# Performance work log

Measured on AMD Instinct MI355X. Metric: run time of the kernel, lower is better.

## Reference

```python
import jax, jax.numpy as jnp
import numpy as np

B, T, C = 2, 2048, 1024
H = 16
DH = C // H  # 64
EPS = 1e-5


def setup_inputs() -> dict:
    key = jax.random.key(0)
    ks = jax.random.split(key, 12)
    s = lambda k, shape, fan: jax.random.normal(k, shape, jnp.float32) / np.sqrt(fan)
    return {
        'x': jax.random.normal(ks[0], (B, T, C), jnp.float32),
        'wq': s(ks[1], (H, C, DH), C),
        'wk': s(ks[2], (H, C, DH), C),
        'wv': s(ks[3], (H, C, DH), C),
        'w_proj': s(ks[4], (C, C), C),
        'b_proj': jnp.zeros((C,), jnp.float32),
        'g_ln1': jnp.ones((C,), jnp.float32),
        'b_ln1': jnp.zeros((C,), jnp.float32),
        'g_ln2': jnp.ones((C,), jnp.float32),
        'b_ln2': jnp.zeros((C,), jnp.float32),
        'w_ff1': s(ks[5], (C, 4 * C), C),
        'b_ff1': jnp.zeros((4 * C,), jnp.float32),
        'w_ff2': s(ks[6], (4 * C, C), 4 * C),
        'b_ff2': jnp.zeros((C,), jnp.float32),
    }


def _layernorm(x, g, b):
    mu = jnp.mean(x, axis=-1, keepdims=True)
    var = jnp.mean(jnp.square(x - mu), axis=-1, keepdims=True)
    return (x - mu) * jax.lax.rsqrt(var + EPS) * g + b


def _attention(x, wq, wk, wv, w_proj, b_proj):
    # per-head projections, batched over heads: [B,T,C] x [H,C,Dh] -> [B,H,T,Dh]
    q = jnp.einsum('btc,hcd->bhtd', x, wq)
    k = jnp.einsum('btc,hcd->bhtd', x, wk)
    v = jnp.einsum('btc,hcd->bhtd', x, wv)
    scores = jnp.einsum('bhtd,bhsd->bhts', q, k) / np.sqrt(DH).astype(np.float32)
    t = x.shape[1]
    causal = jnp.tril(jnp.ones((t, t), bool))
    scores = jnp.where(causal, scores, -jnp.inf)
    w = jax.nn.softmax(scores, axis=-1)
    out = jnp.einsum('bhts,bhsd->bhtd', w, v)  # [B,H,T,Dh]
    # concat heads (head order matches torch cat over head list)
    out = out.transpose(0, 2, 1, 3).reshape(x.shape[0], t, C)
    return out @ w_proj + b_proj


def reference(x, wq, wk, wv, w_proj, b_proj, g_ln1, b_ln1, g_ln2, b_ln2, w_ff1, b_ff1, w_ff2, b_ff2):
    x = x + _attention(_layernorm(x, g_ln1, b_ln1), wq, wk, wv, w_proj, b_proj)
    h = _layernorm(x, g_ln2, b_ln2)
    ff = jax.nn.relu(h @ w_ff1 + b_ff1) @ w_ff2 + b_ff2
    return x + ff
```

## Files before the change

### kernel.cpp

```cpp
#include <hip/hip_runtime.h>

#define DEV __device__ __forceinline__

typedef __attribute__((ext_vector_type(4))) float f32x4;
typedef __attribute__((ext_vector_type(8))) short short8;
typedef __attribute__((ext_vector_type(8))) __bf16 bf16x8;

DEV unsigned short f2bf(float f) {
  __bf16 h = (__bf16)f;
  return __builtin_bit_cast(unsigned short, h);
}
DEV unsigned pack2(float a, float b) {
  return (unsigned)f2bf(a) | ((unsigned)f2bf(b) << 16);
}
DEV bf16x8 ld_bf8(const unsigned short* p) {
  short8 v = *(const short8*)p;
  return __builtin_bit_cast(bf16x8, v);
}
DEV f32x4 MFMA(bf16x8 a, bf16x8 b, f32x4 c) {
  return __builtin_amdgcn_mfma_f32_16x16x32_bf16(a, b, c, 0, 0, 0);
}

typedef const __attribute__((address_space(1))) void GV;
typedef __attribute__((address_space(3))) void LV;
DEV void gl_lds16(const void* g, void* l) {
  __builtin_amdgcn_global_load_lds((GV*)g, (LV*)l, 16, 0, 0);
}

DEV void xcd_decode(int gx, int& bx, int& by) {
  const int nwg = gridDim.x, bid = blockIdx.x;
  const int cpx = nwg >> 3;
  const int swz = (bid & 7) * cpx + (bid >> 3);
  by = swz / gx;
  bx = swz % gx;
}

template<int RX, int RY, int RCOLS>
DEV void xcd_decode2(int& bx, int& by) {
  const int bid = blockIdx.x;
  const int xcd = bid & 7, local = bid >> 3;
  bx = (xcd % RCOLS) * RX + (local % RX);
  by = (xcd / RCOLS) * RY + (local / RX);
}

__global__ void __launch_bounds__(256) ln_fused(
    const float* __restrict__ x, const float* __restrict__ g,
    const float* __restrict__ b, unsigned short* __restrict__ y)
{
  const int row = blockIdx.x, tid = threadIdx.x;
  const float4 xv = ((const float4*)(x + (size_t)row * 1024))[tid];
  float s  = xv.x + xv.y + xv.z + xv.w;
  float s2 = xv.x * xv.x + xv.y * xv.y + xv.z * xv.z + xv.w * xv.w;
#pragma unroll
  for (int o = 32; o > 0; o >>= 1) { s += __shfl_down(s, o); s2 += __shfl_down(s2, o); }
  __shared__ float ps[4], ps2[4];
  if ((tid & 63) == 0) { ps[tid >> 6] = s; ps2[tid >> 6] = s2; }
  __syncthreads();
  float S  = ps[0] + ps[1] + ps[2] + ps[3];
  float S2 = ps2[0] + ps2[1] + ps2[2] + ps2[3];
  float mu = S * (1.f / 1024.f);
  float rs = rsqrtf(S2 * (1.f / 1024.f) - mu * mu + 1e-5f);
  const float4 gv = ((const float4*)g)[tid];
  const float4 bv = ((const float4*)b)[tid];
  uint2 r;
  r.x = pack2((xv.x - mu) * rs * gv.x + bv.x, (xv.y - mu) * rs * gv.y + bv.y);
  r.y = pack2((xv.z - mu) * rs * gv.z + bv.z, (xv.w - mu) * rs * gv.w + bv.w);
  ((uint2*)(y + (size_t)row * 1024))[tid] = r;
}

__global__ void __launch_bounds__(256) transp_f2b(
    const float* __restrict__ src, unsigned short* __restrict__ dst, int R, int C)
{
  __shared__ float t[64][65];
  const int c0 = blockIdx.x * 64, r0 = blockIdx.y * 64;
  const int tx = threadIdx.x & 63, tq = threadIdx.x >> 6;
#pragma unroll
  for (int i = 0; i < 16; i++) {
    int r = tq * 16 + i;
    t[r][tx] = src[(size_t)(r0 + r) * C + c0 + tx];
  }
  __syncthreads();
#pragma unroll
  for (int i = 0; i < 16; i++) {
    int c = tq * 16 + i;
    dst[(size_t)(c0 + c) * R + r0 + tx] = f2bf(t[tx][c]);
  }
}

__global__ void __launch_bounds__(256) qkv_transp(
    const float* __restrict__ wq, const float* __restrict__ wk,
    const float* __restrict__ wv, unsigned short* __restrict__ dst)
{
  __shared__ float t[64][65];
  const int c0 = blockIdx.x * 64, h = blockIdx.y, z = blockIdx.z;
  const float* w = (z == 0 ? wq : z == 1 ? wk : wv) + (size_t)h * 1024 * 64;
  const int tx = threadIdx.x & 63, tq = threadIdx.x >> 6;
#pragma unroll
  for (int i = 0; i < 16; i++) {
    int c = tq * 16 + i;
    t[c][tx] = w[(size_t)(c0 + c) * 64 + tx];
  }
  __syncthreads();
  unsigned short* drow = dst + (size_t)(z * 1024 + h * 64) * 1024 + c0;
#pragma unroll
  for (int i = 0; i < 16; i++) {
    int d = tq * 16 + i;
    drow[(size_t)d * 1024 + tx] = f2bf(t[tx][d]);
  }
}

__global__ void __launch_bounds__(256) v_transp(
    const unsigned short* __restrict__ qkv, unsigned short* __restrict__ vt)
{
  __shared__ unsigned s[64][65];
  const int t0 = blockIdx.x * 64, h = blockIdx.y, b = blockIdx.z;
  const int tx = threadIdx.x & 63, tq = threadIdx.x >> 6;
#pragma unroll
  for (int i = 0; i < 16; i++) {
    int tr = tq * 16 + i;
    s[tr][tx] = qkv[(size_t)(b * 2048 + t0 + tr) * 3072 + 2048 + h * 64 + tx];
  }
  __syncthreads();
  unsigned short* vb = vt + (size_t)((b * 16 + h) * 64) * 2048 + t0;
#pragma unroll
  for (int i = 0; i < 16; i++) {
    int d = tq * 16 + i;
    vb[(size_t)d * 2048 + tx] = (unsigned short)s[tx][d];
  }
}

template<int BIAS, int RELU, int RES, int OBF, int RX, int RY, int RCOLS>
__global__ void __launch_bounds__(256) gemm_bt(
    const unsigned short* __restrict__ A, const unsigned short* __restrict__ Bt,
    const float* __restrict__ bias, const float* __restrict__ res,
    void* __restrict__ out, int M, int N, int K)
{
  __shared__ unsigned short As[2][128 * 32];
  __shared__ unsigned short Bs[2][128 * 32];
  int bx, by;
  xcd_decode2<RX, RY, RCOLS>(bx, by);
  const int tid = threadIdx.x;
  const int wid = tid >> 6, lane = tid & 63;
  const int lg = lane >> 4, lr = lane & 15;
  const int m0 = by * 128, n0 = bx * 128;
  const int wr = (wid >> 1) * 64, wc = (wid & 1) * 64;

  const int srow = tid >> 2;
  const int scs = (tid & 3) ^ (srow & 3);
  const unsigned short* ga = A + (size_t)(m0 + srow) * K + scs * 8;
  const unsigned short* gb = Bt + (size_t)(n0 + srow) * K + scs * 8;
  const int ca = (lg ^ (lr & 3)) * 8;

  f32x4 acc[4][4] = {};

  auto stage = [&](int buf, int k0) {
    char* asb = (char*)&As[buf][0] + wid * 1024;
    char* bsb = (char*)&Bs[buf][0] + wid * 1024;
    gl_lds16(ga + k0, asb);
    gl_lds16(ga + k0 + (size_t)64 * K, asb + 4096);
    gl_lds16(gb + k0, bsb);
    gl_lds16(gb + k0 + (size_t)64 * K, bsb + 4096);
  };

  stage(0, 0);
  int cur = 0;
  for (int k0 = 0; k0 < K; k0 += 32) {
    __syncthreads();
    if (k0 + 32 < K) stage(cur ^ 1, k0 + 32);
    bf16x8 a[4], b[4];
#pragma unroll
    for (int m = 0; m < 4; m++) a[m] = ld_bf8(&As[cur][(wr + m * 16 + lr) * 32 + ca]);
#pragma unroll
    for (int n = 0; n < 4; n++) b[n] = ld_bf8(&Bs[cur][(wc + n * 16 + lr) * 32 + ca]);
#pragma unroll
    for (int m = 0; m < 4; m++)
#pragma unroll
      for (int n = 0; n < 4; n++)
        acc[m][n] = MFMA(a[m], b[n], acc[m][n]);
    cur ^= 1;
  }

#pragma unroll
  for (int m = 0; m < 4; m++) {
    const int row0 = m0 + wr + m * 16 + lg * 4;
#pragma unroll
    for (int n = 0; n < 4; n++) {
      const int col = n0 + wc + n * 16 + lr;
      const float bv = BIAS ? bias[col] : 0.f;
#pragma unroll
      for (int r = 0; r < 4; r++) {
        const size_t off = (size_t)(row0 + r) * N + col;
        float v = acc[m][n][r] + bv;
        if (RES) v += res[off];
        if (RELU) v = v > 0.f ? v : 0.f;
        if (OBF) ((unsigned short*)out)[off] = f2bf(v);
        else     ((float*)out)[off] = v;
      }
    }
  }
}

template<int BIAS, int RELU, int RES, int OBF, int RX, int RY, int RCOLS>
__global__ void __launch_bounds__(256) gemm_64(
    const unsigned short* __restrict__ A, const unsigned short* __restrict__ Bt,
    const float* __restrict__ bias, const float* __restrict__ res,
    void* __restrict__ out, int M, int N, int K)
{
  __shared__ unsigned short As[2][64 * 64];
  __shared__ unsigned short Bs[2][64 * 64];
  int bx, by;
  xcd_decode2<RX, RY, RCOLS>(bx, by);
  const int tid = threadIdx.x;
  const int wid = tid >> 6, lane = tid & 63;
  const int lg = lane >> 4, lr = lane & 15;
  const int m0 = by * 64, n0 = bx * 64;
  const int wr = (wid >> 1) * 32, wc = (wid & 1) * 32;

  const int srow = tid >> 3;
  const int scs = (tid & 7) ^ (srow & 7);
  const unsigned short* ga = A + (size_t)(m0 + srow) * K + scs * 8;
  const unsigned short* gb = Bt + (size_t)(n0 + srow) * K + scs * 8;
  const int lxs = lr & 7;

  f32x4 acc[2][2] = {};

  auto stage = [&](int buf, int k0) {
    char* asb = (char*)&As[buf][0] + wid * 1024;
    char* bsb = (char*)&Bs[buf][0] + wid * 1024;
    gl_lds16(ga + k0, asb);
    gl_lds16(ga + k0 + (size_t)32 * K, asb + 4096);
    gl_lds16(gb + k0, bsb);
    gl_lds16(gb + k0 + (size_t)32 * K, bsb + 4096);
  };

  stage(0, 0);
  int cur = 0;
  for (int k0 = 0; k0 < K; k0 += 64) {
    __syncthreads();
    if (k0 + 64 < K) stage(cur ^ 1, k0 + 64);
#pragma unroll
    for (int kk = 0; kk < 2; kk++) {
      const int cb = kk * 4;
      bf16x8 a[2], b[2];
#pragma unroll
      for (int m = 0; m < 2; m++)
        a[m] = ld_bf8(&As[cur][(wr + m * 16 + lr) * 64 + ((cb + lg) ^ lxs) * 8]);
#pragma unroll
      for (int n = 0; n < 2; n++)
        b[n] = ld_bf8(&Bs[cur][(wc + n * 16 + lr) * 64 + ((cb + lg) ^ lxs) * 8]);
#pragma unroll
      for (int m = 0; m < 2; m++)
#pragma unroll
        for (int n = 0; n < 2; n++)
          acc[m][n] = MFMA(a[m], b[n], acc[m][n]);
    }
    cur ^= 1;
  }

#pragma unroll
  for (int m = 0; m < 2; m++) {
    const int row0 = m0 + wr + m * 16 + lg * 4;
#pragma unroll
    for (int n = 0; n < 2; n++) {
      const int col = n0 + wc + n * 16 + lr;
      const float bv = BIAS ? bias[col] : 0.f;
#pragma unroll
      for (int r = 0; r < 4; r++) {
        const size_t off = (size_t)(row0 + r) * N + col;
        float v = acc[m][n][r] + bv;
        if (RES) v += res[off];
        if (RELU) v = v > 0.f ? v : 0.f;
        if (OBF) ((unsigned short*)out)[off] = f2bf(v);
        else     ((float*)out)[off] = v;
      }
    }
  }
}

__global__ void __launch_bounds__(256) attn_fwd(
    const unsigned short* __restrict__ qkv, const unsigned short* __restrict__ vt,
    unsigned short* __restrict__ out)
{
  __shared__ unsigned short Ks[2][64 * 64];
  __shared__ unsigned short Vs[2][64 * 64];
  __shared__ unsigned short PA[4][16][72];
  __shared__ unsigned short PB[4][16][72];

  int j, bh;
  xcd_decode(16, j, bh);
  const int b = bh >> 4, h = bh & 15;
  const int tid = threadIdx.x, wid = tid >> 6, lane = tid & 63;
  const int lg = lane >> 4, lr = lane & 15;

  const int tA = j, tB = 31 - j;
  const int nkt = tB + 1;
  const float C2 = 0.18033688f;

  const unsigned short* kbase = qkv + (size_t)(b * 2048) * 3072 + 1024 + h * 64;
  const unsigned short* vbase = vt + (size_t)(bh * 64) * 2048;

  const int sr = tid >> 3;
  const int sc = tid & 7;
  const int c0 = sc ^ (sr & 7);

  auto stage = [&](int buf, int kt) {
    const int kv0 = kt * 64;
    char* kd = (char*)&Ks[buf][0] + wid * 1024;
    char* vd = (char*)&Vs[buf][0] + wid * 1024;
    gl_lds16(kbase + (size_t)(kv0 + sr) * 3072 + c0 * 8, kd);
    gl_lds16(kbase + (size_t)(kv0 + 32 + sr) * 3072 + c0 * 8, kd + 4096);
    gl_lds16(vbase + (size_t)sr * 2048 + kv0 + c0 * 8, vd);
    gl_lds16(vbase + (size_t)(32 + sr) * 2048 + kv0 + c0 * 8, vd + 4096);
  };

  auto process = [&](int kt, int qt, const bf16x8& qf0, const bf16x8& qf1,
                     f32x4 (&o)[4], float& l, int buf, unsigned short* Pr) {
    const int kv0 = kt * 64;
    const int qg = qt * 64 + wid * 16 + lr;
    const unsigned short* Kb = &Ks[buf][0];
    const unsigned short* Vb = &Vs[buf][0];
    f32x4 s[4] = {};
    __builtin_amdgcn_s_setprio(1);
#pragma unroll
    for (int f = 0; f < 4; f++) {
      const int row = f * 16 + lr;
      const int rc = row & 7;
      s[f] = MFMA(ld_bf8(Kb + row * 64 + (lg ^ rc) * 8), qf0, s[f]);
      s[f] = MFMA(ld_bf8(Kb + row * 64 + ((lg | 4) ^ rc) * 8), qf1, s[f]);
    }
    __builtin_amdgcn_s_setprio(0);
    float p[16];
    const bool diag = (kt == qt);
    float ps = 0.f;
#pragma unroll
    for (int f = 0; f < 4; f++)
#pragma unroll
      for (int r = 0; r < 4; r++) {
        float sv = s[f][r];
        if (diag) {
          const int kv = kv0 + f * 16 + lg * 4 + r;
          sv = (kv <= qg) ? sv : -1e30f;
        }
        const float pv = exp2f(sv * C2);
        p[f * 4 + r] = pv;
        ps += pv;
      }
    l += ps;
#pragma unroll
    for (int f = 0; f < 4; f++) {
      *(unsigned*)(Pr + f * 16 + lg * 4)     = pack2(p[f * 4 + 0], p[f * 4 + 1]);
      *(unsigned*)(Pr + f * 16 + lg * 4 + 2) = pack2(p[f * 4 + 2], p[f * 4 + 3]);
    }
    const bf16x8 pf0 = ld_bf8(Pr + lg * 8);
    const bf16x8 pf1 = ld_bf8(Pr + 32 + lg * 8);
    __builtin_amdgcn_s_setprio(1);
#pragma unroll
    for (int df = 0; df < 4; df++) {
      const int row = df * 16 + lr;
      const int rc = row & 7;
      o[df] = MFMA(ld_bf8(Vb + row * 64 + (lg ^ rc) * 8), pf0, o[df]);
      o[df] = MFMA(ld_bf8(Vb + row * 64 + ((lg | 4) ^ rc) * 8), pf1, o[df]);
    }
    __builtin_amdgcn_s_setprio(0);
  };

  const unsigned short* qb = qkv + (size_t)(b * 2048) * 3072 + h * 64;
  const int qrA = tA * 64 + wid * 16 + lr;
  const int qrB = tB * 64 + wid * 16 + lr;
  const bf16x8 qA0 = ld_bf8(qb + (size_t)qrA * 3072 + lg * 8);
  const bf16x8 qA1 = ld_bf8(qb + (size_t)qrA * 3072 + 32 + lg * 8);
  const bf16x8 qB0 = ld_bf8(qb + (size_t)qrB * 3072 + lg * 8);
  const bf16x8 qB1 = ld_bf8(qb + (size_t)qrB * 3072 + 32 + lg * 8);

  f32x4 oA[4] = {}, oB[4] = {};
  float lA = 0.f, lB = 0.f;

  stage(0, 0);
  __syncthreads();
  for (int kt = 0; kt < nkt; kt++) {
    const int buf = kt & 1;
    if (kt + 1 < nkt) stage(buf ^ 1, kt + 1);
    if (kt <= tA) process(kt, tA, qA0, qA1, oA, lA, buf, &PA[wid][lr][0]);
    process(kt, tB, qB0, qB1, oB, lB, buf, &PB[wid][lr][0]);
    __syncthreads();
  }

  lA += __shfl_xor(lA, 16); lA += __shfl_xor(lA, 32);
  lB += __shfl_xor(lB, 16); lB += __shfl_xor(lB, 32);
  const float invA = 1.f / lA, invB = 1.f / lB;
  {
    const int qg = tA * 64 + wid * 16 + lr;
    unsigned* orow = (unsigned*)(out + (size_t)(b * 2048 + qg) * 1024 + h * 64 + lg * 4);
#pragma unroll
    for (int df = 0; df < 4; df++) {
      orow[df * 8 + 0] = pack2(oA[df][0] * invA, oA[df][1] * invA);
      orow[df * 8 + 1] = pack2(oA[df][2] * invA, oA[df][3] * invA);
    }
  }
  {
    const int qg = tB * 64 + wid * 16 + lr;
    unsigned* orow = (unsigned*)(out + (size_t)(b * 2048 + qg) * 1024 + h * 64 + lg * 4);
#pragma unroll
    for (int df = 0; df < 4; df++) {
      orow[df * 8 + 0] = pack2(oB[df][0] * invB, oB[df][1] * invB);
      orow[df * 8 + 1] = pack2(oB[df][2] * invB, oB[df][3] * invB);
    }
  }
}

extern "C" void kernel_launch(void* const* d_in, const int* in_sizes, int n_in,
                              void* d_out, int out_size, void* d_ws, size_t ws_size,
                              hipStream_t stream)
{
  const float* x     = (const float*)d_in[0];
  const float* wq    = (const float*)d_in[1];
  const float* wk    = (const float*)d_in[2];
  const float* wv    = (const float*)d_in[3];
  const float* wproj = (const float*)d_in[4];
  const float* bproj = (const float*)d_in[5];
  const float* gln1  = (const float*)d_in[6];
  const float* bln1  = (const float*)d_in[7];
  const float* gln2  = (const float*)d_in[8];
  const float* bln2  = (const float*)d_in[9];
  const float* wff1  = (const float*)d_in[10];
  const float* bff1  = (const float*)d_in[11];
  const float* wff2  = (const float*)d_in[12];
  const float* bff2  = (const float*)d_in[13];

  char* ws = (char*)d_ws;
  const size_t MB = 1u << 20;
  float*          x2    = (float*)         (ws + 0 * MB);
  unsigned short* hbuf  = (unsigned short*)(ws + 16 * MB);
  unsigned short* xn1   = (unsigned short*)(ws + 24 * MB);
  unsigned short* attn  = (unsigned short*)(ws + 24 * MB);
  unsigned short* qkvb  = (unsigned short*)(ws + 32 * MB);
  unsigned short* vtb   = (unsigned short*)(ws + 56 * MB);
  unsigned short* a1    = (unsigned short*)(ws + 32 * MB);
  unsigned short* wqkvT = (unsigned short*)(ws + 64 * MB);
  unsigned short* wprojT= (unsigned short*)(ws + 70 * MB);
  unsigned short* wff1T = (unsigned short*)(ws + 72 * MB);
  unsigned short* wff2T = (unsigned short*)(ws + 80 * MB);

  qkv_transp<<<dim3(16, 16, 3), 256, 0, stream>>>(wq, wk, wv, wqkvT);
  transp_f2b<<<dim3(16, 16), 256, 0, stream>>>(wproj, wprojT, 1024, 1024);
  transp_f2b<<<dim3(64, 16), 256, 0, stream>>>(wff1, wff1T, 1024, 4096);
  transp_f2b<<<dim3(16, 64), 256, 0, stream>>>(wff2, wff2T, 4096, 1024);

  ln_fused<<<4096, 256, 0, stream>>>(x, gln1, bln1, xn1);
  gemm_bt<0, 0, 0, 1, 12, 8, 2><<<768, 256, 0, stream>>>(
      xn1, wqkvT, nullptr, nullptr, qkvb, 4096, 3072, 1024);
  v_transp<<<dim3(32, 16, 2), 256, 0, stream>>>(qkvb, vtb);
  attn_fwd<<<512, 256, 0, stream>>>(qkvb, vtb, attn);
  gemm_64<1, 0, 1, 0, 8, 16, 2><<<1024, 256, 0, stream>>>(
      attn, wprojT, bproj, x, x2, 4096, 1024, 1024);
  ln_fused<<<4096, 256, 0, stream>>>(x2, gln2, bln2, hbuf);
  gemm_bt<1, 1, 0, 1, 8, 16, 4><<<1024, 256, 0, stream>>>(
      hbuf, wff1T, bff1, nullptr, a1, 4096, 4096, 1024);
  gemm_64<1, 0, 1, 0, 8, 16, 2><<<1024, 256, 0, stream>>>(
      a1, wff2T, bff2, x2, (float*)d_out, 4096, 1024, 4096);
}
```

Before: 235.2 us.

## Split attention query tiles across 8 waves instead of 4 waves each doing two

The attention kernel now launches 512 threads per block. Waves 0-3 handle the early query tile and waves 4-7 handle the mirrored late tile, where before each of 4 waves processed both tiles serially. K/V staging is spread over 8 waves, so each thread issues half as many loads. Waves on the short tile sit idle at the barriers once their causal range ends, and per-block register and LDS pressure changes, which may affect occupancy.

```diff
diff --git a/kernel.cpp b/kernel.cpp
--- a/kernel.cpp
+++ b/kernel.cpp
@@ -277,14 +277,13 @@
   }
 }
 
-__global__ void __launch_bounds__(256) attn_fwd(
+__global__ void __launch_bounds__(512) attn_fwd(
     const unsigned short* __restrict__ qkv, const unsigned short* __restrict__ vt,
     unsigned short* __restrict__ out)
 {
   __shared__ unsigned short Ks[2][64 * 64];
   __shared__ unsigned short Vs[2][64 * 64];
-  __shared__ unsigned short PA[4][16][72];
-  __shared__ unsigned short PB[4][16][72];
+  __shared__ unsigned short PW[8][16][72];
 
   int j, bh;
   xcd_decode(16, j, bh);
@@ -294,6 +293,7 @@
 
   const int tA = j, tB = 31 - j;
   const int nkt = tB + 1;
+  const int qt = (wid >= 4) ? tB : tA;
   const float C2 = 0.18033688f;
 
   const unsigned short* kbase = qkv + (size_t)(b * 2048) * 3072 + 1024 + h * 64;
@@ -308,103 +308,82 @@
     char* kd = (char*)&Ks[buf][0] + wid * 1024;
     char* vd = (char*)&Vs[buf][0] + wid * 1024;
     gl_lds16(kbase + (size_t)(kv0 + sr) * 3072 + c0 * 8, kd);
-    gl_lds16(kbase + (size_t)(kv0 + 32 + sr) * 3072 + c0 * 8, kd + 4096);
     gl_lds16(vbase + (size_t)sr * 2048 + kv0 + c0 * 8, vd);
-    gl_lds16(vbase + (size_t)(32 + sr) * 2048 + kv0 + c0 * 8, vd + 4096);
   };
 
-  auto process = [&](int kt, int qt, const bf16x8& qf0, const bf16x8& qf1,
-                     f32x4 (&o)[4], float& l, int buf, unsigned short* Pr) {
-    const int kv0 = kt * 64;
-    const int qg = qt * 64 + wid * 16 + lr;
-    const unsigned short* Kb = &Ks[buf][0];
-    const unsigned short* Vb = &Vs[buf][0];
-    f32x4 s[4] = {};
-    __builtin_amdgcn_s_setprio(1);
-#pragma unroll
-    for (int f = 0; f < 4; f++) {
-      const int row = f * 16 + lr;
-      const int rc = row & 7;
-      s[f] = MFMA(ld_bf8(Kb + row * 64 + (lg ^ rc) * 8), qf0, s[f]);
-      s[f] = MFMA(ld_bf8(Kb + row * 64 + ((lg | 4) ^ rc) * 8), qf1, s[f]);
-    }
-    __builtin_amdgcn_s_setprio(0);
-    float p[16];
-    const bool diag = (kt == qt);
-    float ps = 0.f;
-#pragma unroll
-    for (int f = 0; f < 4; f++)
-#pragma unroll
-      for (int r = 0; r < 4; r++) {
-        float sv = s[f][r];
-        if (diag) {
-          const int kv = kv0 + f * 16 + lg * 4 + r;
-          sv = (kv <= qg) ? sv : -1e30f;
-        }
-        const float pv = exp2f(sv * C2);
-        p[f * 4 + r] = pv;
-        ps += pv;
-      }
-    l += ps;
-#pragma unroll
-    for (int f = 0; f < 4; f++) {
-      *(unsigned*)(Pr + f * 16 + lg * 4)     = pack2(p[f * 4 + 0], p[f * 4 + 1]);
-      *(unsigned*)(Pr + f * 16 + lg * 4 + 2) = pack2(p[f * 4 + 2], p[f * 4 + 3]);
-    }
-    const bf16x8 pf0 = ld_bf8(Pr + lg * 8);
-    const bf16x8 pf1 = ld_bf8(Pr + 32 + lg * 8);
-    __builtin_amdgcn_s_setprio(1);
-#pragma unroll
-    for (int df = 0; df < 4; df++) {
-      const int row = df * 16 + lr;
-      const int rc = row & 7;
-      o[df] = MFMA(ld_bf8(Vb + row * 64 + (lg ^ rc) * 8), pf0, o[df]);
-      o[df] = MFMA(ld_bf8(Vb + row * 64 + ((lg | 4) ^ rc) * 8), pf1, o[df]);
-    }
-    __builtin_amdgcn_s_setprio(0);
-  };
-
   const unsigned short* qb = qkv + (size_t)(b * 2048) * 3072 + h * 64;
-  const int qrA = tA * 64 + wid * 16 + lr;
-  const int qrB = tB * 64 + wid * 16 + lr;
-  const bf16x8 qA0 = ld_bf8(qb + (size_t)qrA * 3072 + lg * 8);
-  const bf16x8 qA1 = ld_bf8(qb + (size_t)qrA * 3072 + 32 + lg * 8);
-  const bf16x8 qB0 = ld_bf8(qb + (size_t)qrB * 3072 + lg * 8);
-  const bf16x8 qB1 = ld_bf8(qb + (size_t)qrB * 3072 + 32 + lg * 8);
-
-  f32x4 oA[4] = {}, oB[4] = {};
-  float lA = 0.f, lB = 0.f;
+  const int qg = qt * 64 + (wid & 3) * 16 + lr;
+  const bf16x8 qf0 = ld_bf8(qb + (size_t)qg * 3072 + lg * 8);
+  const bf16x8 qf1 = ld_bf8(qb + (size_t)qg * 3072 + 32 + lg * 8);
+
+  f32x4 o[4] = {};
+  float l = 0.f;
+  unsigned short* Pr = &PW[wid][lr][0];
 
   stage(0, 0);
   __syncthreads();
   for (int kt = 0; kt < nkt; kt++) {
     const int buf = kt & 1;
     if (kt + 1 < nkt) stage(buf ^ 1, kt + 1);
-    if (kt <= tA) process(kt, tA, qA0, qA1, oA, lA, buf, &PA[wid][lr][0]);
-    process(kt, tB, qB0, qB1, oB, lB, buf, &PB[wid][lr][0]);
+    if (kt <= qt) {
+      const int kv0 = kt * 64;
+      const unsigned short* Kb = &Ks[buf][0];
+      const unsigned short* Vb = &Vs[buf][0];
+      f32x4 s[4] = {};
+      __builtin_amdgcn_s_setprio(1);
+#pragma unroll
+      for (int f = 0; f < 4; f++) {
+        const int row = f * 16 + lr;
+        const int rc = row & 7;
+        s[f] = MFMA(ld_bf8(Kb + row * 64 + (lg ^ rc) * 8), qf0, s[f]);
+        s[f] = MFMA(ld_bf8(Kb + row * 64 + ((lg | 4) ^ rc) * 8), qf1, s[f]);
+      }
+      __builtin_amdgcn_s_setprio(0);
+      float p[16];
+      const bool diag = (kt == qt);
+      float ps = 0.f;
+#pragma unroll
+      for (int f = 0; f < 4; f++)
+#pragma unroll
+        for (int r = 0; r < 4; r++) {
+          float sv = s[f][r];
+          if (diag) {
+            const int kv = kv0 + f * 16 + lg * 4 + r;
+            sv = (kv <= qg) ? sv : -1e30f;
+          }
+          const float pv = exp2f(sv * C2);
+          p[f * 4 + r] = pv;
+          ps += pv;
+        }
+      l += ps;
+#pragma unroll
+      for (int f = 0; f < 4; f++) {
+        *(unsigned*)(Pr + f * 16 + lg * 4)     = pack2(p[f * 4 + 0], p[f * 4 + 1]);
+        *(unsigned*)(Pr + f * 16 + lg * 4 + 2) = pack2(p[f * 4 + 2], p[f * 4 + 3]);
+      }
+      const bf16x8 pf0 = ld_bf8(Pr + lg * 8);
+      const bf16x8 pf1 = ld_bf8(Pr + 32 + lg * 8);
+      __builtin_amdgcn_s_setprio(1);
+#pragma unroll
+      for (int df = 0; df < 4; df++) {
+        const int row = df * 16 + lr;
+        const int rc = row & 7;
+        o[df] = MFMA(ld_bf8(Vb + row * 64 + (lg ^ rc) * 8), pf0, o[df]);
+        o[df] = MFMA(ld_bf8(Vb + row * 64 + ((lg | 4) ^ rc) * 8), pf1, o[df]);
+      }
+      __builtin_amdgcn_s_setprio(0);
+    }
     __syncthreads();
   }
 
-  lA += __shfl_xor(lA, 16); lA += __shfl_xor(lA, 32);
-  lB += __shfl_xor(lB, 16); lB += __shfl_xor(lB, 32);
-  const float invA = 1.f / lA, invB = 1.f / lB;
-  {
-    const int qg = tA * 64 + wid * 16 + lr;
-    unsigned* orow = (unsigned*)(out + (size_t)(b * 2048 + qg) * 1024 + h * 64 + lg * 4);
-#pragma unroll
-    for (int df = 0; df < 4; df++) {
-      orow[df * 8 + 0] = pack2(oA[df][0] * invA, oA[df][1] * invA);
-      orow[df * 8 + 1] = pack2(oA[df][2] * invA, oA[df][3] * invA);
-    }
-  }
-  {
-    const int qg = tB * 64 + wid * 16 + lr;
-    unsigned* orow = (unsigned*)(out + (size_t)(b * 2048 + qg) * 1024 + h * 64 + lg * 4);
-#pragma unroll
-    for (int df = 0; df < 4; df++) {
-      orow[df * 8 + 0] = pack2(oB[df][0] * invB, oB[df][1] * invB);
-      orow[df * 8 + 1] = pack2(oB[df][2] * invB, oB[df][3] * invB);
-    }
+  l += __shfl_xor(l, 16);
+  l += __shfl_xor(l, 32);
+  const float inv = 1.f / l;
+  unsigned* orow = (unsigned*)(out + (size_t)(b * 2048 + qg) * 1024 + h * 64 + lg * 4);
+#pragma unroll
+  for (int df = 0; df < 4; df++) {
+    orow[df * 8 + 0] = pack2(o[df][0] * inv, o[df][1] * inv);
+    orow[df * 8 + 1] = pack2(o[df][2] * inv, o[df][3] * inv);
   }
 }
 
@@ -450,7 +429,7 @@
   gemm_bt<0, 0, 0, 1, 12, 8, 2><<<768, 256, 0, stream>>>(
       xn1, wqkvT, nullptr, nullptr, qkvb, 4096, 3072, 1024);
   v_transp<<<dim3(32, 16, 2), 256, 0, stream>>>(qkvb, vtb);
-  attn_fwd<<<512, 256, 0, stream>>>(qkvb, vtb, attn);
+  attn_fwd<<<512, 512, 0, stream>>>(qkvb, vtb, attn);
   gemm_64<1, 0, 1, 0, 8, 16, 2><<<1024, 256, 0, stream>>>(
       attn, wprojT, bproj, x, x2, 4096, 1024, 1024);
   ln_fused<<<4096, 256, 0, stream>>>(x2, gln2, bln2, hbuf);
```

Result: no change. 237.4 us (+0.9%).
